# Performance work log

Hardware: AMD Instinct MI355X
Metric: run time of the kernel (lower is better)

The kernel has to match this reference:

```python
import jax, jax.numpy as jnp
import numpy as np

B, S, H, DK, DV = 4, 1024, 12, 64, 64
DM = H * DK  # 768
NEG = -1e12


def setup_inputs() -> dict:
    key = jax.random.key(0)
    ks = jax.random.split(key, 16)
    sc = 0.02
    return {
        "q": jax.random.normal(ks[0], (B, S, DM), jnp.float32),
        "k": jax.random.normal(ks[1], (B, S, DM), jnp.float32),
        "v": jax.random.normal(ks[2], (B, S, DM), jnp.float32),
        "attention_mask": jnp.zeros((1, 1, S, S), jnp.float32),
        "position_bias": jax.random.normal(ks[3], (S, S, DK), jnp.float32) * sc,
        "v_mask": jax.random.randint(ks[4], (B, S), 0, 2, jnp.int32),
        "Wq": jax.random.normal(ks[5], (DM, H * DK), jnp.float32) * sc,
        "bq": jnp.zeros((H * DK,), jnp.float32),
        "Wk": jax.random.normal(ks[6], (DM, H * DK), jnp.float32) * sc,
        "bk": jnp.zeros((H * DK,), jnp.float32),
        "Wv": jax.random.normal(ks[7], (DM, H * DV), jnp.float32) * sc,
        "bv": jnp.zeros((H * DV,), jnp.float32),
        "Wo": jax.random.normal(ks[8], (H * DV, DM), jnp.float32) * sc,
        "bo": jnp.zeros((DM,), jnp.float32),
    }


def reference(q, k, v, attention_mask, position_bias, v_mask,
              Wq, bq, Wk, bk, Wv, bv, Wo, bo):
    b, s, _ = q.shape
    qw = (q @ Wq + bq).reshape(b, s, H, DK)
    kw = (k @ Wk + bk).reshape(b, s, H, DK)
    vw = (v @ Wv + bv).reshape(b, s, H, DV)
    # scores with relative position bias (NEZHA-style)
    a = jnp.einsum('bjhd,bkhd->bhjk', qw, kw)
    a = a + jnp.einsum('bjhd,jkd->bhjk', qw, position_bias)
    a = a / jnp.sqrt(jnp.float32(DK))
    a = a + attention_mask
    # sequence mask on key axis: x*m + NEG*(1-m)
    m = v_mask.astype(a.dtype)[:, None, None, :]
    a = a * m + NEG * (1.0 - m)
    A = jax.nn.softmax(a, axis=-1)
    attn = jnp.einsum('bhjk,bkhd->bjhd', A, vw)
    attn = attn + jnp.einsum('bhjk,jkd->bjhd', A, position_bias)
    out = attn.reshape(b, s, H * DV) @ Wo + bo
    return out
```

## Files before the change

kernel.cpp:

```cpp
#include <hip/hip_runtime.h>
#include <hip/hip_bf16.h>
#include <hip/hip_fp16.h>

#define NS 1024
#define NB 4
#define NH 12
#define NDM 768
#define NBH 48

typedef __attribute__((ext_vector_type(8))) short bf16x8;
typedef __attribute__((ext_vector_type(4))) float f32x4;

__device__ __forceinline__ ushort f2b(float f){
  uint u = __float_as_uint(f);
  u += 0x7fffu + ((u >> 16) & 1u);
  return (ushort)(u >> 16);
}
__device__ __forceinline__ float b2f(ushort s){ return __uint_as_float(((uint)s) << 16); }
__device__ __forceinline__ ushort f2h(float f){
  __half h = __float2half(f); ushort u; __builtin_memcpy(&u, &h, 2); return u;
}
__device__ __forceinline__ float h2f(ushort u){
  __half h; __builtin_memcpy(&h, &u, 2); return __half2float(h);
}
__device__ __forceinline__ f32x4 mfma16(bf16x8 a, bf16x8 b, f32x4 c){
  return __builtin_amdgcn_mfma_f32_16x16x32_bf16(a, b, c, 0, 0, 0);
}

__global__ void k_cvt(const float* __restrict__ src, ushort* __restrict__ dst, int n){
  int i = (blockIdx.x * blockDim.x + threadIdx.x) * 4;
  if (i >= n) return;
  float4 v = *(const float4*)(src + i);
  ushort4 o; o.x = f2b(v.x); o.y = f2b(v.y); o.z = f2b(v.z); o.w = f2b(v.w);
  *(ushort4*)(dst + i) = o;
}

__global__ void k_wT(const float* __restrict__ W, ushort* __restrict__ WT, float scale){
  __shared__ float tl[32][33];
  int bx = blockIdx.x * 32, by = blockIdx.y * 32;
  int tx = threadIdx.x, ty = threadIdx.y;
  #pragma unroll
  for (int r = 0; r < 32; r += 8) tl[ty + r][tx] = W[(by + ty + r) * NDM + bx + tx];
  __syncthreads();
  #pragma unroll
  for (int r = 0; r < 32; r += 8) WT[(bx + ty + r) * NDM + by + tx] = f2b(tl[tx][ty + r] * scale);
}

template<int OUT_F32>
__global__ __launch_bounds__(256) void k_gemm768(const ushort* __restrict__ A,
    const ushort* __restrict__ Bt, const float* __restrict__ bias, float bscale,
    void* __restrict__ out){
  __shared__ ushort As[128][72];
  __shared__ ushort Bs[128][72];
  int m0 = blockIdx.x * 128, n0 = blockIdx.y * 128;
  int t = threadIdx.x, w = t >> 6, l = t & 63;
  int wm = (w >> 1) * 64, wn = (w & 1) * 64;
  f32x4 acc[4][4] = {};
  for (int k0 = 0; k0 < 768; k0 += 64){
    __syncthreads();
    #pragma unroll
    for (int it = 0; it < 4; ++it){
      int idx = it * 256 + t, r = idx >> 3, c = (idx & 7) * 8;
      *(bf16x8*)&As[r][c] = *(const bf16x8*)(A + (size_t)(m0 + r) * NDM + k0 + c);
      *(bf16x8*)&Bs[r][c] = *(const bf16x8*)(Bt + (size_t)(n0 + r) * NDM + k0 + c);
    }
    __syncthreads();
    #pragma unroll
    for (int ks = 0; ks < 2; ++ks){
      bf16x8 af[4], bfm[4];
      #pragma unroll
      for (int mt = 0; mt < 4; ++mt) af[mt] = *(const bf16x8*)&As[wm + mt*16 + (l & 15)][ks*32 + (l >> 4) * 8];
      #pragma unroll
      for (int nt = 0; nt < 4; ++nt) bfm[nt] = *(const bf16x8*)&Bs[wn + nt*16 + (l & 15)][ks*32 + (l >> 4) * 8];
      #pragma unroll
      for (int mt = 0; mt < 4; ++mt)
        #pragma unroll
        for (int nt = 0; nt < 4; ++nt)
          acc[mt][nt] = mfma16(af[mt], bfm[nt], acc[mt][nt]);
    }
  }
  #pragma unroll
  for (int mt = 0; mt < 4; ++mt)
    #pragma unroll
    for (int nt = 0; nt < 4; ++nt){
      int col = n0 + wn + nt * 16 + (l & 15);
      float bv = bias[col] * bscale;
      #pragma unroll
      for (int i = 0; i < 4; ++i){
        int row = m0 + wm + mt * 16 + (l >> 4) * 4 + i;
        float vv = acc[mt][nt][i] + bv;
        if (OUT_F32) ((float*)out)[(size_t)row * NDM + col] = vv;
        else ((ushort*)out)[(size_t)row * NDM + col] = f2b(vv);
      }
    }
}

__global__ void k_vT(const ushort* __restrict__ vw, ushort* __restrict__ vwT){
  __shared__ ushort tl[64][72];
  int s0 = blockIdx.x * 64, bh = blockIdx.y;
  int b = bh / NH, h = bh % NH;
  int t = threadIdx.x;
  #pragma unroll
  for (int it = 0; it < 2; ++it){
    int idx = it * 256 + t, r = idx >> 3, c = (idx & 7) * 8;
    *(bf16x8*)&tl[r][c] = *(const bf16x8*)(vw + ((size_t)(b * NS) + s0 + r) * NDM + h * 64 + c);
  }
  __syncthreads();
  #pragma unroll
  for (int it = 0; it < 16; ++it){
    int idx = it * 256 + t, d = idx >> 6, s = idx & 63;
    vwT[((size_t)bh * 64 + d) * NS + s0 + s] = tl[s][d];
  }
}

__global__ __launch_bounds__(256) void k_qk(const ushort* __restrict__ qwp,
    const ushort* __restrict__ kwp, ushort* __restrict__ Sqk){
  __shared__ ushort As[128][72];
  __shared__ ushort Bs[128][72];
  int j0 = blockIdx.x * 128, k0 = blockIdx.y * 128, bh = blockIdx.z;
  int b = bh / NH, h = bh % NH;
  int t = threadIdx.x, w = t >> 6, l = t & 63;
  int wm = (w >> 1) * 64, wn = (w & 1) * 64;
  #pragma unroll
  for (int it = 0; it < 4; ++it){
    int idx = it * 256 + t, r = idx >> 3, c = (idx & 7) * 8;
    *(bf16x8*)&As[r][c] = *(const bf16x8*)(qwp + ((size_t)(b * NS) + j0 + r) * NDM + h * 64 + c);
    *(bf16x8*)&Bs[r][c] = *(const bf16x8*)(kwp + ((size_t)(b * NS) + k0 + r) * NDM + h * 64 + c);
  }
  __syncthreads();
  f32x4 acc[4][4] = {};
  #pragma unroll
  for (int ks = 0; ks < 2; ++ks){
    bf16x8 af[4], bfm[4];
    #pragma unroll
    for (int mt = 0; mt < 4; ++mt) af[mt] = *(const bf16x8*)&As[wm + mt*16 + (l & 15)][ks*32 + (l >> 4) * 8];
    #pragma unroll
    for (int nt = 0; nt < 4; ++nt) bfm[nt] = *(const bf16x8*)&Bs[wn + nt*16 + (l & 15)][ks*32 + (l >> 4) * 8];
    #pragma unroll
    for (int mt = 0; mt < 4; ++mt)
      #pragma unroll
      for (int nt = 0; nt < 4; ++nt)
        acc[mt][nt] = mfma16(af[mt], bfm[nt], acc[mt][nt]);
  }
  #pragma unroll
  for (int mt = 0; mt < 4; ++mt)
    #pragma unroll
    for (int nt = 0; nt < 4; ++nt)
      #pragma unroll
      for (int i = 0; i < 4; ++i){
        int jj = j0 + wm + mt * 16 + (l >> 4) * 4 + i;
        int kk = k0 + wn + nt * 16 + (l & 15);
        Sqk[((size_t)bh * NS + jj) * NS + kk] = f2b(acc[mt][nt][i]);
      }
}

__global__ __launch_bounds__(512) void k_attnrow(const ushort* __restrict__ qw,
    ushort* __restrict__ SqkA, const float* __restrict__ pb,
    const float* __restrict__ amask, const int* __restrict__ vmask,
    float* __restrict__ outpb){
  __shared__ ushort SA[48][1032];
  __shared__ ushort PBs[18432];
  __shared__ ushort QWs[48][72];
  int j = blockIdx.x;
  int t = threadIdx.x, w = t >> 6, l = t & 63;
  if (t < 384){
    int bh = t >> 3, c = (t & 7) * 8;
    int b = bh / NH, h = bh % NH;
    *(bf16x8*)&QWs[bh][c] = *(const bf16x8*)(qw + ((size_t)(b * NS) + j) * NDM + h * 64 + c);
  }
  for (int kc = 0; kc < 4; ++kc){
    __syncthreads();
    #pragma unroll
    for (int it = 0; it < 8; ++it){
      int idx = it * 512 + t;
      int kk = idx >> 4, c4 = (idx & 15) * 4;
      float4 pv = *(const float4*)(pb + ((size_t)j * NS + kc * 256 + kk) * 64 + c4);
      ushort4 o; o.x = f2b(pv.x); o.y = f2b(pv.y); o.z = f2b(pv.z); o.w = f2b(pv.w);
      *(ushort4*)&PBs[kk * 72 + c4] = o;
    }
    __syncthreads();
    f32x4 acc[3][2] = {};
    #pragma unroll
    for (int ks = 0; ks < 2; ++ks){
      bf16x8 af[3], bfm[2];
      #pragma unroll
      for (int mt = 0; mt < 3; ++mt) af[mt] = *(const bf16x8*)&QWs[mt*16 + (l & 15)][ks*32 + (l >> 4) * 8];
      #pragma unroll
      for (int nt = 0; nt < 2; ++nt) bfm[nt] = *(const bf16x8*)&PBs[(w*32 + nt*16 + (l & 15)) * 72 + ks*32 + (l >> 4) * 8];
      #pragma unroll
      for (int mt = 0; mt < 3; ++mt)
        #pragma unroll
        for (int nt = 0; nt < 2; ++nt)
          acc[mt][nt] = mfma16(af[mt], bfm[nt], acc[mt][nt]);
    }
    #pragma unroll
    for (int nt = 0; nt < 2; ++nt){
      int kg = kc * 256 + w * 32 + nt * 16 + (l & 15);
      float am = amask[j * NS + kg];
      #pragma unroll
      for (int mt = 0; mt < 3; ++mt)
        #pragma unroll
        for (int i = 0; i < 4; ++i){
          int bh = mt * 16 + (l >> 4) * 4 + i;
          int b = bh / NH;
          float sv = acc[mt][nt][i] + b2f(SqkA[((size_t)bh * NS + j) * NS + kg]) + am;
          sv = vmask[b * NS + kg] ? sv : -60000.0f;
          SA[bh][kg] = f2h(sv);
        }
    }
  }
  __syncthreads();
  for (int r = 0; r < 6; ++r){
    int bh = w * 6 + r;
    uint raw[8]; float sv[16];
    #pragma unroll
    for (int rr = 0; rr < 8; ++rr) raw[rr] = *(const uint*)&SA[bh][rr * 128 + l * 2];
    #pragma unroll
    for (int rr = 0; rr < 8; ++rr){
      sv[rr*2]   = h2f((ushort)(raw[rr] & 0xffffu));
      sv[rr*2+1] = h2f((ushort)(raw[rr] >> 16));
    }
    float mx = -1e30f;
    #pragma unroll
    for (int ii = 0; ii < 16; ++ii) mx = fmaxf(mx, sv[ii]);
    #pragma unroll
    for (int off = 32; off > 0; off >>= 1) mx = fmaxf(mx, __shfl_xor(mx, off));
    float p[16], sum = 0.f;
    #pragma unroll
    for (int ii = 0; ii < 16; ++ii){ p[ii] = __expf(sv[ii] - mx); sum += p[ii]; }
    #pragma unroll
    for (int off = 32; off > 0; off >>= 1) sum += __shfl_xor(sum, off);
    float inv = 1.0f / sum;
    size_t gbase = ((size_t)bh * NS + j) * NS;
    #pragma unroll
    for (int rr = 0; rr < 8; ++rr){
      uint pk = (uint)f2b(p[rr*2] * inv) | ((uint)f2b(p[rr*2+1] * inv) << 16);
      *(uint*)&SA[bh][rr * 128 + l * 2] = pk;
      *(uint*)((ushort*)SqkA + gbase + rr * 128 + l * 2) = pk;
    }
  }
  f32x4 opb[2] = {};
  int ntl = (w < 4) ? 2 : 1;
  for (int kc = 0; kc < 4; ++kc){
    __syncthreads();
    for (int it = 0; it < 32; ++it){
      int idx = it * 512 + t;
      int kk = idx >> 6, d = idx & 63;
      PBs[d * 264 + kk] = f2b(pb[((size_t)j * NS + kc * 256 + kk) * 64 + d]);
    }
    __syncthreads();
    for (int tt = 0; tt < ntl; ++tt){
      int tau = w + tt * 8, mt = tau >> 2, nt = tau & 3;
      #pragma unroll
      for (int ks = 0; ks < 8; ++ks){
        bf16x8 af  = *(const bf16x8*)&SA[mt*16 + (l & 15)][kc*256 + ks*32 + (l >> 4) * 8];
        bf16x8 bfm = *(const bf16x8*)&PBs[(nt*16 + (l & 15)) * 264 + ks*32 + (l >> 4) * 8];
        opb[tt] = mfma16(af, bfm, opb[tt]);
      }
    }
  }
  for (int tt = 0; tt < ntl; ++tt){
    int tau = w + tt * 8, mt = tau >> 2, nt = tau & 3;
    #pragma unroll
    for (int i = 0; i < 4; ++i){
      int bh = mt * 16 + (l >> 4) * 4 + i, d = nt * 16 + (l & 15);
      outpb[((size_t)j * NBH + bh) * 64 + d] = opb[tt][i];
    }
  }
}

__global__ __launch_bounds__(256) void k_pv(const ushort* __restrict__ Abuf,
    const ushort* __restrict__ vwT, const float* __restrict__ outpb,
    ushort* __restrict__ attn){
  __shared__ ushort As[128][72];
  __shared__ ushort Bs[64][72];
  int j0 = blockIdx.x * 128, bh = blockIdx.y;
  int b = bh / NH, h = bh % NH;
  int t = threadIdx.x, w = t >> 6, l = t & 63;
  f32x4 acc[2][4] = {};
  for (int k0 = 0; k0 < NS; k0 += 64){
    __syncthreads();
    #pragma unroll
    for (int it = 0; it < 4; ++it){
      int idx = it * 256 + t, r = idx >> 3, c = (idx & 7) * 8;
      *(bf16x8*)&As[r][c] = *(const bf16x8*)(Abuf + ((size_t)bh * NS + j0 + r) * NS + k0 + c);
    }
    #pragma unroll
    for (int it = 0; it < 2; ++it){
      int idx = it * 256 + t, r = idx >> 3, c = (idx & 7) * 8;
      *(bf16x8*)&Bs[r][c] = *(const bf16x8*)(vwT + ((size_t)bh * 64 + r) * NS + k0 + c);
    }
    __syncthreads();
    #pragma unroll
    for (int ks = 0; ks < 2; ++ks){
      bf16x8 af[2], bfm[4];
      #pragma unroll
      for (int mt = 0; mt < 2; ++mt) af[mt] = *(const bf16x8*)&As[w*32 + mt*16 + (l & 15)][ks*32 + (l >> 4) * 8];
      #pragma unroll
      for (int nt = 0; nt < 4; ++nt) bfm[nt] = *(const bf16x8*)&Bs[nt*16 + (l & 15)][ks*32 + (l >> 4) * 8];
      #pragma unroll
      for (int mt = 0; mt < 2; ++mt)
        #pragma unroll
        for (int nt = 0; nt < 4; ++nt)
          acc[mt][nt] = mfma16(af[mt], bfm[nt], acc[mt][nt]);
    }
  }
  #pragma unroll
  for (int mt = 0; mt < 2; ++mt)
    #pragma unroll
    for (int nt = 0; nt < 4; ++nt)
      #pragma unroll
      for (int i = 0; i < 4; ++i){
        int jj = j0 + w * 32 + mt * 16 + (l >> 4) * 4 + i;
        int d = nt * 16 + (l & 15);
        float vv = acc[mt][nt][i] + outpb[((size_t)jj * NBH + bh) * 64 + d];
        attn[((size_t)(b * NS) + jj) * NDM + h * 64 + d] = f2b(vv);
      }
}

extern "C" void kernel_launch(void* const* d_in, const int* in_sizes, int n_in,
                              void* d_out, int out_size, void* d_ws, size_t ws_size,
                              hipStream_t stream) {
  const float* q     = (const float*)d_in[0];
  const float* k     = (const float*)d_in[1];
  const float* v     = (const float*)d_in[2];
  const float* amask = (const float*)d_in[3];
  const float* pb    = (const float*)d_in[4];
  const int*   vmask = (const int*)d_in[5];
  const float* Wq    = (const float*)d_in[6];
  const float* bq    = (const float*)d_in[7];
  const float* Wk    = (const float*)d_in[8];
  const float* bk    = (const float*)d_in[9];
  const float* Wv    = (const float*)d_in[10];
  const float* bv    = (const float*)d_in[11];
  const float* Wo    = (const float*)d_in[12];
  const float* bo    = (const float*)d_in[13];
  float* out = (float*)d_out;

  char* ws = (char*)d_ws;
  const size_t SZ_T  = (size_t)NB * NS * NDM * 2;
  const size_t SZ_WT = (size_t)NDM * NDM * 2;
  const size_t SZ_S  = (size_t)NBH * NS * NS * 2;
  size_t off = 0;
  ushort* qbf  = (ushort*)(ws + off); off += SZ_T;
  ushort* kbf  = (ushort*)(ws + off); off += SZ_T;
  ushort* vbf  = (ushort*)(ws + off); off += SZ_T;
  ushort* WqT  = (ushort*)(ws + off); off += SZ_WT;
  ushort* WkT  = (ushort*)(ws + off); off += SZ_WT;
  ushort* WvT  = (ushort*)(ws + off); off += SZ_WT;
  ushort* WoT  = (ushort*)(ws + off); off += SZ_WT;
  ushort* qwp  = (ushort*)(ws + off); off += SZ_T;
  ushort* kwp  = (ushort*)(ws + off); off += SZ_T;
  ushort* vwp  = (ushort*)(ws + off); off += SZ_T;
  ushort* Sqk  = (ushort*)(ws + off); off += SZ_S;
  float*  opb  = (float*)(ws + off);  off += (size_t)NS * NBH * 64 * 4;
  ushort* vwT  = kbf;
  ushort* attn = qbf;

  const int nElem = NB * NS * NDM;
  k_cvt<<<dim3(nElem / 1024), dim3(256), 0, stream>>>(q, qbf, nElem);
  k_cvt<<<dim3(nElem / 1024), dim3(256), 0, stream>>>(k, kbf, nElem);
  k_cvt<<<dim3(nElem / 1024), dim3(256), 0, stream>>>(v, vbf, nElem);
  k_wT<<<dim3(24, 24), dim3(32, 8), 0, stream>>>(Wq, WqT, 0.125f);
  k_wT<<<dim3(24, 24), dim3(32, 8), 0, stream>>>(Wk, WkT, 1.0f);
  k_wT<<<dim3(24, 24), dim3(32, 8), 0, stream>>>(Wv, WvT, 1.0f);
  k_wT<<<dim3(24, 24), dim3(32, 8), 0, stream>>>(Wo, WoT, 1.0f);
  k_gemm768<0><<<dim3(32, 6), dim3(256), 0, stream>>>(kbf, WkT, bk, 1.0f, kwp);
  k_gemm768<0><<<dim3(32, 6), dim3(256), 0, stream>>>(qbf, WqT, bq, 0.125f, qwp);
  k_gemm768<0><<<dim3(32, 6), dim3(256), 0, stream>>>(vbf, WvT, bv, 1.0f, vwp);
  k_vT<<<dim3(16, NBH), dim3(256), 0, stream>>>(vwp, vwT);
  k_qk<<<dim3(8, 8, NBH), dim3(256), 0, stream>>>(qwp, kwp, Sqk);
  k_attnrow<<<dim3(NS), dim3(512), 0, stream>>>(qwp, Sqk, pb, amask, vmask, opb);
  k_pv<<<dim3(8, NBH), dim3(256), 0, stream>>>(Sqk, vwT, opb, attn);
  k_gemm768<1><<<dim3(32, 6), dim3(256), 0, stream>>>(attn, WoT, bo, 1.0f, out);
}
```

Before: 662.3 us.

## Stream attention rows in chunks with deferred normalization and batch prep kernels

The per-row attention kernel now processes keys in 128-wide chunks. The row max comes from the first chunk only, and unnormalized bf16 probabilities are written back, so the large shared score buffer and the separate softmax pass go away. The 1/sum factor is applied later in the position-bias output and in the PV kernel. The score buffer layout changes to [j][bh][k] to suit row access, and the conversion, weight-transpose and Q/K/V projection launches are merged into single grid-indexed launches. The first-chunk max plus a clamp at 30 in the exponent is an approximation that could lose accuracy if later chunks hold much larger scores.

```diff
diff --git a/kernel.cpp b/kernel.cpp
--- a/kernel.cpp
+++ b/kernel.cpp
@@ -7,6 +7,7 @@
 #define NH 12
 #define NDM 768
 #define NBH 48
+#define CHK 128
 
 typedef __attribute__((ext_vector_type(8))) short bf16x8;
 typedef __attribute__((ext_vector_type(4))) float f32x4;
@@ -17,42 +18,48 @@
   return (ushort)(u >> 16);
 }
 __device__ __forceinline__ float b2f(ushort s){ return __uint_as_float(((uint)s) << 16); }
-__device__ __forceinline__ ushort f2h(float f){
-  __half h = __float2half(f); ushort u; __builtin_memcpy(&u, &h, 2); return u;
-}
-__device__ __forceinline__ float h2f(ushort u){
-  __half h; __builtin_memcpy(&h, &u, 2); return __half2float(h);
-}
 __device__ __forceinline__ f32x4 mfma16(bf16x8 a, bf16x8 b, f32x4 c){
   return __builtin_amdgcn_mfma_f32_16x16x32_bf16(a, b, c, 0, 0, 0);
 }
 
-__global__ void k_cvt(const float* __restrict__ src, ushort* __restrict__ dst, int n){
-  int i = (blockIdx.x * blockDim.x + threadIdx.x) * 4;
-  if (i >= n) return;
-  float4 v = *(const float4*)(src + i);
-  ushort4 o; o.x = f2b(v.x); o.y = f2b(v.y); o.z = f2b(v.z); o.w = f2b(v.w);
-  *(ushort4*)(dst + i) = o;
-}
-
-__global__ void k_wT(const float* __restrict__ W, ushort* __restrict__ WT, float scale){
+__global__ void k_cvt3(const float* __restrict__ q, const float* __restrict__ k,
+                       const float* __restrict__ v, ushort* __restrict__ qo,
+                       ushort* __restrict__ ko, ushort* __restrict__ vo){
+  int i = (blockIdx.x * 256 + threadIdx.x) * 4;
+  const float* s = blockIdx.y == 0 ? q : (blockIdx.y == 1 ? k : v);
+  ushort* d      = blockIdx.y == 0 ? qo : (blockIdx.y == 1 ? ko : vo);
+  float4 x = *(const float4*)(s + i);
+  ushort4 o; o.x = f2b(x.x); o.y = f2b(x.y); o.z = f2b(x.z); o.w = f2b(x.w);
+  *(ushort4*)(d + i) = o;
+}
+
+__global__ void k_wT4(const float* __restrict__ Wq, const float* __restrict__ Wk,
+                      const float* __restrict__ Wv, const float* __restrict__ Wo,
+                      ushort* __restrict__ Tq, ushort* __restrict__ Tk,
+                      ushort* __restrict__ Tv, ushort* __restrict__ To){
   __shared__ float tl[32][33];
+  const float* W; ushort* T; float sc = 1.0f;
+  switch (blockIdx.z){
+    case 0:  W = Wq; T = Tq; sc = 0.125f; break;
+    case 1:  W = Wk; T = Tk; break;
+    case 2:  W = Wv; T = Tv; break;
+    default: W = Wo; T = To; break;
+  }
   int bx = blockIdx.x * 32, by = blockIdx.y * 32;
   int tx = threadIdx.x, ty = threadIdx.y;
   #pragma unroll
   for (int r = 0; r < 32; r += 8) tl[ty + r][tx] = W[(by + ty + r) * NDM + bx + tx];
   __syncthreads();
   #pragma unroll
-  for (int r = 0; r < 32; r += 8) WT[(bx + ty + r) * NDM + by + tx] = f2b(tl[tx][ty + r] * scale);
+  for (int r = 0; r < 32; r += 8) T[(bx + ty + r) * NDM + by + tx] = f2b(tl[tx][ty + r] * sc);
 }
 
 template<int OUT_F32>
-__global__ __launch_bounds__(256) void k_gemm768(const ushort* __restrict__ A,
+__device__ __forceinline__ void gemm768_body(const ushort* __restrict__ A,
     const ushort* __restrict__ Bt, const float* __restrict__ bias, float bscale,
-    void* __restrict__ out){
+    void* __restrict__ out, int m0, int n0){
   __shared__ ushort As[128][72];
   __shared__ ushort Bs[128][72];
-  int m0 = blockIdx.x * 128, n0 = blockIdx.y * 128;
   int t = threadIdx.x, w = t >> 6, l = t & 63;
   int wm = (w >> 1) * 64, wn = (w & 1) * 64;
   f32x4 acc[4][4] = {};
@@ -93,6 +100,25 @@
         else ((ushort*)out)[(size_t)row * NDM + col] = f2b(vv);
       }
     }
+}
+
+__global__ __launch_bounds__(256) void k_proj3(
+    const ushort* __restrict__ qb, const ushort* __restrict__ kb, const ushort* __restrict__ vb,
+    const ushort* __restrict__ Tq, const ushort* __restrict__ Tk, const ushort* __restrict__ Tv,
+    const float* __restrict__ bq, const float* __restrict__ bk, const float* __restrict__ bv,
+    ushort* __restrict__ qo, ushort* __restrict__ ko, ushort* __restrict__ vo){
+  const ushort *A, *Bt; const float* bias; ushort* out; float bscale = 1.0f;
+  switch (blockIdx.z){
+    case 0:  A = qb; Bt = Tq; bias = bq; out = qo; bscale = 0.125f; break;
+    case 1:  A = kb; Bt = Tk; bias = bk; out = ko; break;
+    default: A = vb; Bt = Tv; bias = bv; out = vo; break;
+  }
+  gemm768_body<0>(A, Bt, bias, bscale, out, blockIdx.x * 128, blockIdx.y * 128);
+}
+
+__global__ __launch_bounds__(256) void k_outproj(const ushort* __restrict__ A,
+    const ushort* __restrict__ Bt, const float* __restrict__ bias, float* __restrict__ out){
+  gemm768_body<1>(A, Bt, bias, 1.0f, out, blockIdx.x * 128, blockIdx.y * 128);
 }
 
 __global__ void k_vT(const ushort* __restrict__ vw, ushort* __restrict__ vwT){
@@ -150,128 +176,181 @@
       for (int i = 0; i < 4; ++i){
         int jj = j0 + wm + mt * 16 + (l >> 4) * 4 + i;
         int kk = k0 + wn + nt * 16 + (l & 15);
-        Sqk[((size_t)bh * NS + jj) * NS + kk] = f2b(acc[mt][nt][i]);
-      }
-}
-
-__global__ __launch_bounds__(512) void k_attnrow(const ushort* __restrict__ qw,
-    ushort* __restrict__ SqkA, const float* __restrict__ pb,
-    const float* __restrict__ amask, const int* __restrict__ vmask,
-    float* __restrict__ outpb){
-  __shared__ ushort SA[48][1032];
-  __shared__ ushort PBs[18432];
+        Sqk[((size_t)jj * NBH + bh) * NS + kk] = f2b(acc[mt][nt][i]);
+      }
+}
+
+__global__ __launch_bounds__(512, 4) void k_attnflash(const ushort* __restrict__ qw,
+    ushort* SqkA, const float* __restrict__ pb, const float* __restrict__ amask,
+    const int* __restrict__ vmask, float* __restrict__ outpb, float* __restrict__ invlg){
+  __shared__ ushort PBrow[CHK][72];
+  __shared__ ushort PBtr[64][136];
+  __shared__ ushort SQs[48][136];
+  __shared__ ushort Pb[48][136];
   __shared__ ushort QWs[48][72];
+  __shared__ float  VMs[4][CHK];
+  __shared__ float  Wred[48][8];
+  __shared__ float  RowM[48];
+  __shared__ float  InvL[48];
   int j = blockIdx.x;
   int t = threadIdx.x, w = t >> 6, l = t & 63;
+  int lr = l & 15, lc = l >> 4;
   if (t < 384){
     int bh = t >> 3, c = (t & 7) * 8;
     int b = bh / NH, h = bh % NH;
     *(bf16x8*)&QWs[bh][c] = *(const bf16x8*)(qw + ((size_t)(b * NS) + j) * NDM + h * 64 + c);
   }
-  for (int kc = 0; kc < 4; ++kc){
-    __syncthreads();
-    #pragma unroll
-    for (int it = 0; it < 8; ++it){
-      int idx = it * 512 + t;
-      int kk = idx >> 4, c4 = (idx & 15) * 4;
-      float4 pv = *(const float4*)(pb + ((size_t)j * NS + kc * 256 + kk) * 64 + c4);
-      ushort4 o; o.x = f2b(pv.x); o.y = f2b(pv.y); o.z = f2b(pv.z); o.w = f2b(pv.w);
-      *(ushort4*)&PBs[kk * 72 + c4] = o;
-    }
-    __syncthreads();
-    f32x4 acc[3][2] = {};
-    #pragma unroll
-    for (int ks = 0; ks < 2; ++ks){
-      bf16x8 af[3], bfm[2];
-      #pragma unroll
-      for (int mt = 0; mt < 3; ++mt) af[mt] = *(const bf16x8*)&QWs[mt*16 + (l & 15)][ks*32 + (l >> 4) * 8];
-      #pragma unroll
-      for (int nt = 0; nt < 2; ++nt) bfm[nt] = *(const bf16x8*)&PBs[(w*32 + nt*16 + (l & 15)) * 72 + ks*32 + (l >> 4) * 8];
-      #pragma unroll
-      for (int mt = 0; mt < 3; ++mt)
-        #pragma unroll
-        for (int nt = 0; nt < 2; ++nt)
-          acc[mt][nt] = mfma16(af[mt], bfm[nt], acc[mt][nt]);
-    }
-    #pragma unroll
-    for (int nt = 0; nt < 2; ++nt){
-      int kg = kc * 256 + w * 32 + nt * 16 + (l & 15);
-      float am = amask[j * NS + kg];
-      #pragma unroll
-      for (int mt = 0; mt < 3; ++mt)
-        #pragma unroll
-        for (int i = 0; i < 4; ++i){
-          int bh = mt * 16 + (l >> 4) * 4 + i;
-          int b = bh / NH;
-          float sv = acc[mt][nt][i] + b2f(SqkA[((size_t)bh * NS + j) * NS + kg]) + am;
-          sv = vmask[b * NS + kg] ? sv : -60000.0f;
-          SA[bh][kg] = f2h(sv);
-        }
-    }
-  }
-  __syncthreads();
-  for (int r = 0; r < 6; ++r){
-    int bh = w * 6 + r;
-    uint raw[8]; float sv[16];
-    #pragma unroll
-    for (int rr = 0; rr < 8; ++rr) raw[rr] = *(const uint*)&SA[bh][rr * 128 + l * 2];
-    #pragma unroll
-    for (int rr = 0; rr < 8; ++rr){
-      sv[rr*2]   = h2f((ushort)(raw[rr] & 0xffffu));
-      sv[rr*2+1] = h2f((ushort)(raw[rr] >> 16));
-    }
-    float mx = -1e30f;
-    #pragma unroll
-    for (int ii = 0; ii < 16; ++ii) mx = fmaxf(mx, sv[ii]);
-    #pragma unroll
-    for (int off = 32; off > 0; off >>= 1) mx = fmaxf(mx, __shfl_xor(mx, off));
-    float p[16], sum = 0.f;
-    #pragma unroll
-    for (int ii = 0; ii < 16; ++ii){ p[ii] = __expf(sv[ii] - mx); sum += p[ii]; }
-    #pragma unroll
-    for (int off = 32; off > 0; off >>= 1) sum += __shfl_xor(sum, off);
-    float inv = 1.0f / sum;
-    size_t gbase = ((size_t)bh * NS + j) * NS;
-    #pragma unroll
-    for (int rr = 0; rr < 8; ++rr){
-      uint pk = (uint)f2b(p[rr*2] * inv) | ((uint)f2b(p[rr*2+1] * inv) << 16);
-      *(uint*)&SA[bh][rr * 128 + l * 2] = pk;
-      *(uint*)((ushort*)SqkA + gbase + rr * 128 + l * 2) = pk;
-    }
-  }
+  float lsum[3][4] = {};
+  float mrow[3][4];
   f32x4 opb[2] = {};
   int ntl = (w < 4) ? 2 : 1;
-  for (int kc = 0; kc < 4; ++kc){
-    __syncthreads();
-    for (int it = 0; it < 32; ++it){
+  for (int c = 0; c < NS / CHK; ++c){
+    __syncthreads();
+    const float* pbc = pb + ((size_t)j * NS + c * CHK) * 64;
+    #pragma unroll
+    for (int it = 0; it < 4; ++it){
       int idx = it * 512 + t;
-      int kk = idx >> 6, d = idx & 63;
-      PBs[d * 264 + kk] = f2b(pb[((size_t)j * NS + kc * 256 + kk) * 64 + d]);
-    }
-    __syncthreads();
+      int kk = idx >> 4, d0 = (idx & 15) * 4;
+      float4 pv = *(const float4*)(pbc + (size_t)kk * 64 + d0);
+      ushort4 o; o.x = f2b(pv.x); o.y = f2b(pv.y); o.z = f2b(pv.z); o.w = f2b(pv.w);
+      *(ushort4*)&PBrow[kk][d0] = o;
+    }
+    #pragma unroll
+    for (int it = 0; it < 4; ++it){
+      int idx = it * 512 + t;
+      int d = idx & 63, k4 = (idx >> 6) * 4;
+      ushort4 o;
+      o.x = f2b(pbc[(size_t)(k4 + 0) * 64 + d]);
+      o.y = f2b(pbc[(size_t)(k4 + 1) * 64 + d]);
+      o.z = f2b(pbc[(size_t)(k4 + 2) * 64 + d]);
+      o.w = f2b(pbc[(size_t)(k4 + 3) * 64 + d]);
+      *(ushort4*)&PBtr[d][k4] = o;
+    }
+    #pragma unroll
+    for (int it = 0; it < 2; ++it){
+      int idx = it * 512 + t;
+      if (idx < 768){
+        int r = idx >> 4, c8 = (idx & 15) * 8;
+        *(bf16x8*)&SQs[r][c8] = *(const bf16x8*)(SqkA + ((size_t)j * NBH + r) * NS + c * CHK + c8);
+      }
+    }
+    {
+      int b = t >> 7, kk = t & 127;
+      VMs[b][kk] = vmask[b * NS + c * CHK + kk] ? 0.f : -60000.0f;
+    }
+    __syncthreads();
+    f32x4 acc[3] = {};
+    #pragma unroll
+    for (int ks = 0; ks < 2; ++ks){
+      bf16x8 bfm = *(const bf16x8*)&PBrow[w * 16 + lr][ks * 32 + lc * 8];
+      #pragma unroll
+      for (int mt = 0; mt < 3; ++mt){
+        bf16x8 af = *(const bf16x8*)&QWs[mt * 16 + lr][ks * 32 + lc * 8];
+        acc[mt] = mfma16(af, bfm, acc[mt]);
+      }
+    }
+    int kcl = w * 16 + lr;
+    float am = amask[(size_t)j * NS + c * CHK + kcl];
+    float Sv[3][4];
+    #pragma unroll
+    for (int mt = 0; mt < 3; ++mt)
+      #pragma unroll
+      for (int i = 0; i < 4; ++i){
+        int bh = mt * 16 + lc * 4 + i;
+        Sv[mt][i] = acc[mt][i] + b2f(SQs[bh][kcl]) + am + VMs[bh / NH][kcl];
+      }
+    if (c == 0){
+      float vmx[3][4];
+      #pragma unroll
+      for (int mt = 0; mt < 3; ++mt)
+        #pragma unroll
+        for (int i = 0; i < 4; ++i) vmx[mt][i] = Sv[mt][i];
+      #pragma unroll
+      for (int off = 1; off < 16; off <<= 1)
+        #pragma unroll
+        for (int mt = 0; mt < 3; ++mt)
+          #pragma unroll
+          for (int i = 0; i < 4; ++i) vmx[mt][i] = fmaxf(vmx[mt][i], __shfl_xor(vmx[mt][i], off));
+      if (lr == 0)
+        #pragma unroll
+        for (int mt = 0; mt < 3; ++mt)
+          #pragma unroll
+          for (int i = 0; i < 4; ++i) Wred[mt * 16 + lc * 4 + i][w] = vmx[mt][i];
+      __syncthreads();
+      if (t < 48){
+        float m = Wred[t][0];
+        #pragma unroll
+        for (int ww = 1; ww < 8; ++ww) m = fmaxf(m, Wred[t][ww]);
+        RowM[t] = m;
+      }
+      __syncthreads();
+      #pragma unroll
+      for (int mt = 0; mt < 3; ++mt)
+        #pragma unroll
+        for (int i = 0; i < 4; ++i) mrow[mt][i] = RowM[mt * 16 + lc * 4 + i];
+    }
+    #pragma unroll
+    for (int mt = 0; mt < 3; ++mt)
+      #pragma unroll
+      for (int i = 0; i < 4; ++i){
+        float p = __expf(fminf(Sv[mt][i] - mrow[mt][i], 30.0f));
+        lsum[mt][i] += p;
+        Pb[mt * 16 + lc * 4 + i][kcl] = f2b(p);
+      }
+    __syncthreads();
+    #pragma unroll
+    for (int it = 0; it < 2; ++it){
+      int idx = it * 512 + t;
+      if (idx < 768){
+        int r = idx >> 4, c8 = (idx & 15) * 8;
+        *(bf16x8*)(SqkA + ((size_t)j * NBH + r) * NS + c * CHK + c8) = *(const bf16x8*)&Pb[r][c8];
+      }
+    }
     for (int tt = 0; tt < ntl; ++tt){
-      int tau = w + tt * 8, mt = tau >> 2, nt = tau & 3;
-      #pragma unroll
-      for (int ks = 0; ks < 8; ++ks){
-        bf16x8 af  = *(const bf16x8*)&SA[mt*16 + (l & 15)][kc*256 + ks*32 + (l >> 4) * 8];
-        bf16x8 bfm = *(const bf16x8*)&PBs[(nt*16 + (l & 15)) * 264 + ks*32 + (l >> 4) * 8];
+      int tau = w + tt * 8, mt = tau >> 2, nd = tau & 3;
+      #pragma unroll
+      for (int ks = 0; ks < 4; ++ks){
+        bf16x8 af  = *(const bf16x8*)&Pb[mt * 16 + lr][ks * 32 + lc * 8];
+        bf16x8 bfm = *(const bf16x8*)&PBtr[nd * 16 + lr][ks * 32 + lc * 8];
         opb[tt] = mfma16(af, bfm, opb[tt]);
       }
     }
   }
+  #pragma unroll
+  for (int off = 1; off < 16; off <<= 1)
+    #pragma unroll
+    for (int mt = 0; mt < 3; ++mt)
+      #pragma unroll
+      for (int i = 0; i < 4; ++i) lsum[mt][i] += __shfl_xor(lsum[mt][i], off);
+  __syncthreads();
+  if (lr == 0)
+    #pragma unroll
+    for (int mt = 0; mt < 3; ++mt)
+      #pragma unroll
+      for (int i = 0; i < 4; ++i) Wred[mt * 16 + lc * 4 + i][w] = lsum[mt][i];
+  __syncthreads();
+  if (t < 48){
+    float s = 0.f;
+    #pragma unroll
+    for (int ww = 0; ww < 8; ++ww) s += Wred[t][ww];
+    float inv = 1.0f / s;
+    InvL[t] = inv;
+    invlg[(size_t)j * NBH + t] = inv;
+  }
+  __syncthreads();
   for (int tt = 0; tt < ntl; ++tt){
-    int tau = w + tt * 8, mt = tau >> 2, nt = tau & 3;
+    int tau = w + tt * 8, mt = tau >> 2, nd = tau & 3;
     #pragma unroll
     for (int i = 0; i < 4; ++i){
-      int bh = mt * 16 + (l >> 4) * 4 + i, d = nt * 16 + (l & 15);
-      outpb[((size_t)j * NBH + bh) * 64 + d] = opb[tt][i];
+      int bh = mt * 16 + lc * 4 + i, d = nd * 16 + lr;
+      outpb[((size_t)j * NBH + bh) * 64 + d] = opb[tt][i] * InvL[bh];
     }
   }
 }
 
 __global__ __launch_bounds__(256) void k_pv(const ushort* __restrict__ Abuf,
     const ushort* __restrict__ vwT, const float* __restrict__ outpb,
-    ushort* __restrict__ attn){
+    const float* __restrict__ invl, ushort* __restrict__ attn){
   __shared__ ushort As[128][72];
   __shared__ ushort Bs[64][72];
   int j0 = blockIdx.x * 128, bh = blockIdx.y;
@@ -283,7 +362,7 @@
     #pragma unroll
     for (int it = 0; it < 4; ++it){
       int idx = it * 256 + t, r = idx >> 3, c = (idx & 7) * 8;
-      *(bf16x8*)&As[r][c] = *(const bf16x8*)(Abuf + ((size_t)bh * NS + j0 + r) * NS + k0 + c);
+      *(bf16x8*)&As[r][c] = *(const bf16x8*)(Abuf + ((size_t)(j0 + r) * NBH + bh) * NS + k0 + c);
     }
     #pragma unroll
     for (int it = 0; it < 2; ++it){
@@ -305,6 +384,14 @@
           acc[mt][nt] = mfma16(af[mt], bfm[nt], acc[mt][nt]);
     }
   }
+  float il[2][4];
+  #pragma unroll
+  for (int mt = 0; mt < 2; ++mt)
+    #pragma unroll
+    for (int i = 0; i < 4; ++i){
+      int jj = j0 + w * 32 + mt * 16 + (l >> 4) * 4 + i;
+      il[mt][i] = invl[(size_t)jj * NBH + bh];
+    }
   #pragma unroll
   for (int mt = 0; mt < 2; ++mt)
     #pragma unroll
@@ -313,7 +400,7 @@
       for (int i = 0; i < 4; ++i){
         int jj = j0 + w * 32 + mt * 16 + (l >> 4) * 4 + i;
         int d = nt * 16 + (l & 15);
-        float vv = acc[mt][nt][i] + outpb[((size_t)jj * NBH + bh) * 64 + d];
+        float vv = acc[mt][nt][i] * il[mt][i] + outpb[((size_t)jj * NBH + bh) * 64 + d];
         attn[((size_t)(b * NS) + jj) * NDM + h * 64 + d] = f2b(vv);
       }
 }
@@ -354,23 +441,18 @@
   ushort* vwp  = (ushort*)(ws + off); off += SZ_T;
   ushort* Sqk  = (ushort*)(ws + off); off += SZ_S;
   float*  opb  = (float*)(ws + off);  off += (size_t)NS * NBH * 64 * 4;
+  float*  invl = (float*)(ws + off);  off += (size_t)NS * NBH * 4;
   ushort* vwT  = kbf;
   ushort* attn = qbf;
 
   const int nElem = NB * NS * NDM;
-  k_cvt<<<dim3(nElem / 1024), dim3(256), 0, stream>>>(q, qbf, nElem);
-  k_cvt<<<dim3(nElem / 1024), dim3(256), 0, stream>>>(k, kbf, nElem);
-  k_cvt<<<dim3(nElem / 1024), dim3(256), 0, stream>>>(v, vbf, nElem);
-  k_wT<<<dim3(24, 24), dim3(32, 8), 0, stream>>>(Wq, WqT, 0.125f);
-  k_wT<<<dim3(24, 24), dim3(32, 8), 0, stream>>>(Wk, WkT, 1.0f);
-  k_wT<<<dim3(24, 24), dim3(32, 8), 0, stream>>>(Wv, WvT, 1.0f);
-  k_wT<<<dim3(24, 24), dim3(32, 8), 0, stream>>>(Wo, WoT, 1.0f);
-  k_gemm768<0><<<dim3(32, 6), dim3(256), 0, stream>>>(kbf, WkT, bk, 1.0f, kwp);
-  k_gemm768<0><<<dim3(32, 6), dim3(256), 0, stream>>>(qbf, WqT, bq, 0.125f, qwp);
-  k_gemm768<0><<<dim3(32, 6), dim3(256), 0, stream>>>(vbf, WvT, bv, 1.0f, vwp);
+  k_cvt3<<<dim3(nElem / 1024, 3), dim3(256), 0, stream>>>(q, k, v, qbf, kbf, vbf);
+  k_wT4<<<dim3(24, 24, 4), dim3(32, 8), 0, stream>>>(Wq, Wk, Wv, Wo, WqT, WkT, WvT, WoT);
+  k_proj3<<<dim3(32, 6, 3), dim3(256), 0, stream>>>(qbf, kbf, vbf, WqT, WkT, WvT,
+                                                    bq, bk, bv, qwp, kwp, vwp);
   k_vT<<<dim3(16, NBH), dim3(256), 0, stream>>>(vwp, vwT);
   k_qk<<<dim3(8, 8, NBH), dim3(256), 0, stream>>>(qwp, kwp, Sqk);
-  k_attnrow<<<dim3(NS), dim3(512), 0, stream>>>(qwp, Sqk, pb, amask, vmask, opb);
-  k_pv<<<dim3(8, NBH), dim3(256), 0, stream>>>(Sqk, vwT, opb, attn);
-  k_gemm768<1><<<dim3(32, 6), dim3(256), 0, stream>>>(attn, WoT, bo, 1.0f, out);
-}
+  k_attnflash<<<dim3(NS), dim3(512), 0, stream>>>(qwp, Sqk, pb, amask, vmask, opb, invl);
+  k_pv<<<dim3(8, NBH), dim3(256), 0, stream>>>(Sqk, vwT, opb, invl, attn);
+  k_outproj<<<dim3(32, 6), dim3(256), 0, stream>>>(attn, WoT, bo, out);
+}
```

Result: no change. 674.9 us (+1.9%).
